# Optimization experiments

Measured on AMD Instinct MI355X. Metric: run time of the kernel, lower is better.

The kernel has to match this reference:

```python
import jax, jax.numpy as jnp
import numpy as np

ALPHA = 1.702   # SwiGLU alpha (module default)
LIMIT = 7.0     # SwiGLU clamp limit (module default)
EPS = 1e-6      # RMSNorm eps
K = 4           # experts_per_token


def setup_inputs() -> dict:
    key = jax.random.key(0)
    k0, k1, k2, k3 = jax.random.split(key, 4)
    B, S, H, I2, E = 4, 2048, 1536, 6144, 16  # I2 = 2*intermediate_size
    x = jax.random.normal(k0, (B, S, H), dtype=jnp.float32)
    norm_scale = jnp.ones((H,), dtype=jnp.float32)
    gate_w = jax.random.normal(k1, (E, H), dtype=jnp.float32) * 0.02
    w_up = jax.random.normal(k2, (E, I2, H), dtype=jnp.float32) * 0.02
    b_up = jnp.zeros((E, I2), dtype=jnp.float32)
    w_down = jax.random.normal(k3, (E, H, I2 // 2), dtype=jnp.float32) * 0.02
    b_down = jnp.zeros((E, H), dtype=jnp.float32)
    return {"x": x, "norm_scale": norm_scale, "gate_w": gate_w,
            "w_up": w_up, "b_up": b_up, "w_down": w_down, "b_down": b_down}


def _swiglu(h):
    g, l = jnp.split(h, 2, axis=-1)
    g = jnp.minimum(g, LIMIT)
    l = jnp.clip(l, -LIMIT, LIMIT)
    return g * jax.nn.sigmoid(ALPHA * g) * (l + 1.0)


def reference(x, norm_scale, gate_w, w_up, b_up, w_down, b_down):
    E = gate_w.shape[0]
    # RMSNorm (fp32 math)
    var = jnp.mean(x * x, axis=-1, keepdims=True)
    xn = x * jax.lax.rsqrt(var + EPS) * norm_scale  # [B,S,H]
    # Router: top-k over expert logits, softmax over the k logits
    logits = jnp.einsum('bsh,eh->bse', xn, gate_w)  # [B,S,E]
    top_v, top_i = jax.lax.top_k(logits, K)
    probs = jax.nn.softmax(top_v, axis=-1)          # [B,S,K]
    out = jnp.zeros_like(x)
    for i in range(K):
        # Faithful to source: expert id taken from token [0,0], applied to whole batch
        eid = top_i[0, 0, i] % E
        wu = jnp.take(w_up, eid, axis=0)    # [2I, H]
        bu = jnp.take(b_up, eid, axis=0)    # [2I]
        wd = jnp.take(w_down, eid, axis=0)  # [H, I]
        bd = jnp.take(b_down, eid, axis=0)  # [H]
        h = jnp.einsum('bsh,ih->bsi', xn, wu) + bu   # [B,S,2I]
        act = _swiglu(h)                              # [B,S,I]
        eo = jnp.einsum('bsi,hi->bsh', act, wd) + bd  # [B,S,H]
        out = out + probs[:, :, i:i + 1] * eo
    return x + out
```

## Files before the change

### kernel.cpp

```cpp
#include <hip/hip_runtime.h>
#include <hip/hip_bf16.h>
#include <stdint.h>

constexpr int T  = 4 * 2048;
constexpr int H  = 1536;
constexpr int I2 = 6144;
constexpr int II = 3072;
constexpr int EE = 16;
#define ALPHA_ 1.702f
#define LIMIT_ 7.0f
#define EPS_   1e-6f

typedef unsigned short u16;
typedef __bf16 bf16x8 __attribute__((ext_vector_type(8)));
typedef float  f32x4  __attribute__((ext_vector_type(4)));

__device__ __forceinline__ u16 f2bf(float f) {
  union { float f; unsigned int u; } c; c.f = f;
  unsigned int u = c.u + 0x7fffu + ((c.u >> 16) & 1u);
  return (u16)(u >> 16);
}
__device__ __forceinline__ unsigned int pack2(float lo, float hi) {
  return (unsigned int)f2bf(lo) | ((unsigned int)f2bf(hi) << 16);
}

__device__ __forceinline__ void async16(const void* g, void* l) {
  __builtin_amdgcn_global_load_lds(
      (const __attribute__((address_space(1))) unsigned int*)(uintptr_t)g,
      (__attribute__((address_space(3))) unsigned int*)(unsigned int)(uintptr_t)l,
      16, 0, 0);
}

__global__ __launch_bounds__(256) void k_rms_router(
    const float* __restrict__ x, const float* __restrict__ nscale,
    const float* __restrict__ gw, u16* __restrict__ xnb,
    float* __restrict__ logits) {
  const int t = blockIdx.x;
  const int tid = threadIdx.x;
  const int lane = tid & 63, wid = tid >> 6;
  const float* xr = x + (size_t)t * H;
  float v[6]; float ss = 0.f;
#pragma unroll
  for (int j = 0; j < 6; ++j) { v[j] = xr[tid + j * 256]; ss += v[j] * v[j]; }
  __shared__ float red[4];
  for (int off = 32; off; off >>= 1) ss += __shfl_down(ss, off, 64);
  if (lane == 0) red[wid] = ss;
  __syncthreads();
  const float rs = rsqrtf((red[0] + red[1] + red[2] + red[3]) * (1.0f / H) + EPS_);
  float xn[6];
#pragma unroll
  for (int j = 0; j < 6; ++j) {
    const int i = tid + j * 256;
    xn[j] = v[j] * rs * nscale[i];
    xnb[(size_t)t * H + i] = f2bf(xn[j]);
  }
  float acc[16];
#pragma unroll
  for (int e = 0; e < 16; ++e) acc[e] = 0.f;
#pragma unroll
  for (int j = 0; j < 6; ++j) {
    const int i = tid + j * 256;
#pragma unroll
    for (int e = 0; e < 16; ++e) acc[e] += xn[j] * gw[e * H + i];
  }
  __shared__ float lred[4][16];
#pragma unroll
  for (int e = 0; e < 16; ++e) {
    float a = acc[e];
    for (int off = 32; off; off >>= 1) a += __shfl_down(a, off, 64);
    if (lane == 0) lred[wid][e] = a;
  }
  __syncthreads();
  if (tid < 16)
    logits[(size_t)t * 16 + tid] = lred[0][tid] + lred[1][tid] + lred[2][tid] + lred[3][tid];
}

__global__ __launch_bounds__(256) void k_topk(
    const float* __restrict__ logits, float* __restrict__ probs, int* __restrict__ eids) {
  const int t = blockIdx.x * 256 + threadIdx.x;
  if (t >= T) return;
  float v[16];
#pragma unroll
  for (int e = 0; e < 16; ++e) v[e] = logits[(size_t)t * 16 + e];
  float tv[4]; int ti[4]; unsigned used = 0;
#pragma unroll
  for (int j = 0; j < 4; ++j) {
    float best = -3.4e38f; int bi = 0;
#pragma unroll
    for (int e = 0; e < 16; ++e) {
      if (!((used >> e) & 1u) && v[e] > best) { best = v[e]; bi = e; }
    }
    used |= 1u << bi; tv[j] = best; ti[j] = bi;
  }
  const float m = tv[0];
  float ex[4], den = 0.f;
#pragma unroll
  for (int j = 0; j < 4; ++j) { ex[j] = __expf(tv[j] - m); den += ex[j]; }
  const float rden = 1.0f / den;
#pragma unroll
  for (int j = 0; j < 4; ++j) probs[(size_t)t * 4 + j] = ex[j] * rden;
  if (t == 0) {
#pragma unroll
    for (int j = 0; j < 4; ++j) eids[j] = ti[j] % EE;
  }
}

__global__ __launch_bounds__(256) void k_gather_bias(
    const float* __restrict__ bup, const float* __restrict__ bdn,
    const int* __restrict__ eids, float* __restrict__ bu_g, float* __restrict__ bd_g) {
  const int i = blockIdx.x * 256 + threadIdx.x;
  if (i < 4 * I2) {
    const int s = i / I2, r = i - s * I2;
    bu_g[i] = bup[(size_t)eids[s] * I2 + r];
  } else {
    const int j = i - 4 * I2;
    const int s = j / H, r = j - s * H;
    bd_g[j] = bdn[(size_t)eids[s] * H + r];
  }
}

__global__ __launch_bounds__(256) void k_gather_w(
    const float* __restrict__ wup, const float* __restrict__ wdn,
    const int* __restrict__ eids, u16* __restrict__ wu_b, u16* __restrict__ wd_b) {
  const size_t UP = (size_t)4 * I2 * H;
  const size_t u = ((size_t)blockIdx.x * 256 + threadIdx.x) * 8;
  if (u < UP) {
    const int s = (int)(u / ((size_t)I2 * H));
    const size_t r = u - (size_t)s * I2 * H;
    const float4* src = (const float4*)(wup + (size_t)eids[s] * I2 * H + r);
    const float4 a = src[0], b = src[1];
    uint4 o; o.x = pack2(a.x, a.y); o.y = pack2(a.z, a.w);
    o.z = pack2(b.x, b.y); o.w = pack2(b.z, b.w);
    *(uint4*)(wu_b + u) = o;
  } else {
    const size_t q = u - UP;
    const int s = (int)(q / ((size_t)H * II));
    const size_t r = q - (size_t)s * H * II;
    const float4* src = (const float4*)(wdn + (size_t)eids[s] * H * II + r);
    const float4 a = src[0], b = src[1];
    uint4 o; o.x = pack2(a.x, a.y); o.y = pack2(a.z, a.w);
    o.z = pack2(b.x, b.y); o.w = pack2(b.z, b.w);
    *(uint4*)(wd_b + q) = o;
  }
}

__global__ __launch_bounds__(256) void k_gemm1(
    const u16* __restrict__ xnb, const u16* __restrict__ wu_b,
    const float* __restrict__ bu_g, const float* __restrict__ probs,
    u16* __restrict__ act) {
  const int s  = blockIdx.z;
  const int n0 = blockIdx.x * 64;
  const int m0 = blockIdx.y * 128;
  const int tid = threadIdx.x;
  const int lane = tid & 63, wid = tid >> 6;
  const int wm = wid >> 1, wn = wid & 1;
  __shared__ u16 As[128 * 32];
  __shared__ u16 Bg[64 * 32];
  __shared__ u16 Bl[64 * 32];
  const u16* wug = wu_b + (size_t)s * I2 * H;
  f32x4 accg[4][2], accl[4][2];
  const f32x4 z = {0.f, 0.f, 0.f, 0.f};
#pragma unroll
  for (int i = 0; i < 4; ++i)
#pragma unroll
    for (int j = 0; j < 2; ++j) { accg[i][j] = z; accl[i][j] = z; }
  const int row2 = tid >> 2, cg = tid & 3;
  for (int k0 = 0; k0 < H; k0 += 32) {
    async16(xnb + (size_t)(m0 + row2) * H + k0 + cg * 8,        &As[tid * 8]);
    async16(xnb + (size_t)(m0 + 64 + row2) * H + k0 + cg * 8,   &As[2048 + tid * 8]);
    async16(wug + (size_t)(n0 + row2) * H + k0 + cg * 8,        &Bg[tid * 8]);
    async16(wug + (size_t)(II + n0 + row2) * H + k0 + cg * 8,   &Bl[tid * 8]);
    __syncthreads();
    const int quad = (lane >> 4) * 8, r16 = lane & 15;
    bf16x8 a[4], bg[2], bl[2];
#pragma unroll
    for (int i = 0; i < 4; ++i) a[i] = *(const bf16x8*)&As[(wm * 64 + i * 16 + r16) * 32 + quad];
#pragma unroll
    for (int j = 0; j < 2; ++j) {
      bg[j] = *(const bf16x8*)&Bg[(wn * 32 + j * 16 + r16) * 32 + quad];
      bl[j] = *(const bf16x8*)&Bl[(wn * 32 + j * 16 + r16) * 32 + quad];
    }
#pragma unroll
    for (int i = 0; i < 4; ++i)
#pragma unroll
      for (int j = 0; j < 2; ++j) {
        accg[i][j] = __builtin_amdgcn_mfma_f32_16x16x32_bf16(a[i], bg[j], accg[i][j], 0, 0, 0);
        accl[i][j] = __builtin_amdgcn_mfma_f32_16x16x32_bf16(a[i], bl[j], accl[i][j], 0, 0, 0);
      }
    __syncthreads();
  }
  u16* actS = act + (size_t)s * T * II;
  const int crow0 = m0 + wm * 64, ccol0 = n0 + wn * 32;
#pragma unroll
  for (int i = 0; i < 4; ++i) {
#pragma unroll
    for (int j = 0; j < 2; ++j) {
      const int col = ccol0 + j * 16 + (lane & 15);
      const float bug = bu_g[s * I2 + col];
      const float bul = bu_g[s * I2 + II + col];
#pragma unroll
      for (int r = 0; r < 4; ++r) {
        const int row = crow0 + i * 16 + (lane >> 4) * 4 + r;
        float g = accg[i][j][r] + bug;
        float l = accl[i][j][r] + bul;
        g = fminf(g, LIMIT_);
        l = fminf(fmaxf(l, -LIMIT_), LIMIT_);
        const float sig = 1.0f / (1.0f + __expf(-ALPHA_ * g));
        const float a = g * sig * (l + 1.0f);
        const float p = probs[(size_t)row * 4 + s];
        actS[(size_t)row * II + col] = f2bf(a * p);
      }
    }
  }
}

__global__ __launch_bounds__(256) void k_gemm2(
    const u16* __restrict__ act, const u16* __restrict__ wd_b,
    const float* __restrict__ bd_g, const float* __restrict__ probs,
    const float* __restrict__ x, float* __restrict__ out) {
  const int n0 = blockIdx.x * 128;
  const int m0 = blockIdx.y * 128;
  const int tid = threadIdx.x;
  const int lane = tid & 63, wid = tid >> 6;
  const int wm = wid >> 1, wn = wid & 1;
  __shared__ u16 As[128 * 32];
  __shared__ u16 Bs[128 * 32];
  f32x4 acc[4][4];
  const f32x4 z = {0.f, 0.f, 0.f, 0.f};
#pragma unroll
  for (int i = 0; i < 4; ++i)
#pragma unroll
    for (int j = 0; j < 4; ++j) acc[i][j] = z;
  const int row2 = tid >> 2, cg = tid & 3;
  for (int s = 0; s < 4; ++s) {
    const u16* Ab = act + (size_t)s * T * II;
    const u16* Bb = wd_b + (size_t)s * H * II;
    for (int k0 = 0; k0 < II; k0 += 32) {
      async16(Ab + (size_t)(m0 + row2) * II + k0 + cg * 8,      &As[tid * 8]);
      async16(Ab + (size_t)(m0 + 64 + row2) * II + k0 + cg * 8, &As[2048 + tid * 8]);
      async16(Bb + (size_t)(n0 + row2) * II + k0 + cg * 8,      &Bs[tid * 8]);
      async16(Bb + (size_t)(n0 + 64 + row2) * II + k0 + cg * 8, &Bs[2048 + tid * 8]);
      __syncthreads();
      const int quad = (lane >> 4) * 8, r16 = lane & 15;
      bf16x8 a[4], b[4];
#pragma unroll
      for (int i = 0; i < 4; ++i) a[i] = *(const bf16x8*)&As[(wm * 64 + i * 16 + r16) * 32 + quad];
#pragma unroll
      for (int j = 0; j < 4; ++j) b[j] = *(const bf16x8*)&Bs[(wn * 64 + j * 16 + r16) * 32 + quad];
#pragma unroll
      for (int i = 0; i < 4; ++i)
#pragma unroll
        for (int j = 0; j < 4; ++j)
          acc[i][j] = __builtin_amdgcn_mfma_f32_16x16x32_bf16(a[i], b[j], acc[i][j], 0, 0, 0);
      __syncthreads();
    }
  }
#pragma unroll
  for (int i = 0; i < 4; ++i) {
#pragma unroll
    for (int r = 0; r < 4; ++r) {
      const int row = m0 + wm * 64 + i * 16 + (lane >> 4) * 4 + r;
      const float p0 = probs[(size_t)row * 4 + 0], p1 = probs[(size_t)row * 4 + 1];
      const float p2 = probs[(size_t)row * 4 + 2], p3 = probs[(size_t)row * 4 + 3];
#pragma unroll
      for (int j = 0; j < 4; ++j) {
        const int col = n0 + wn * 64 + j * 16 + (lane & 15);
        const float bias = p0 * bd_g[col] + p1 * bd_g[H + col] +
                           p2 * bd_g[2 * H + col] + p3 * bd_g[3 * H + col];
        out[(size_t)row * H + col] = x[(size_t)row * H + col] + acc[i][j][r] + bias;
      }
    }
  }
}

extern "C" void kernel_launch(void* const* d_in, const int* in_sizes, int n_in,
                              void* d_out, int out_size, void* d_ws, size_t ws_size,
                              hipStream_t stream) {
  const float* x      = (const float*)d_in[0];
  const float* nscale = (const float*)d_in[1];
  const float* gw     = (const float*)d_in[2];
  const float* wup    = (const float*)d_in[3];
  const float* bup    = (const float*)d_in[4];
  const float* wdn    = (const float*)d_in[5];
  const float* bdn    = (const float*)d_in[6];
  float* out = (float*)d_out;
  char* ws = (char*)d_ws;
  size_t off = 0;
  auto alloc = [&](size_t bytes) { size_t o = off; off += (bytes + 255) & ~(size_t)255; return o; };
  u16*   xnb    = (u16*)(ws + alloc((size_t)T * H * 2));
  float* logits = (float*)(ws + alloc((size_t)T * 16 * 4));
  float* probs  = (float*)(ws + alloc((size_t)T * 4 * 4));
  int*   eids   = (int*)(ws + alloc(64));
  float* bu_g   = (float*)(ws + alloc((size_t)4 * I2 * 4));
  float* bd_g   = (float*)(ws + alloc((size_t)4 * H * 4));
  u16*   wu_b   = (u16*)(ws + alloc((size_t)4 * I2 * H * 2));
  u16*   wd_b   = (u16*)(ws + alloc((size_t)4 * H * II * 2));
  u16*   act    = (u16*)(ws + alloc((size_t)4 * T * II * 2));
  (void)ws_size; (void)in_sizes; (void)n_in; (void)out_size;

  k_rms_router<<<T, 256, 0, stream>>>(x, nscale, gw, xnb, logits);
  k_topk<<<T / 256, 256, 0, stream>>>(logits, probs, eids);
  k_gather_bias<<<(4 * I2 + 4 * H) / 256, 256, 0, stream>>>(bup, bdn, eids, bu_g, bd_g);
  {
    const size_t total = (size_t)4 * I2 * H + (size_t)4 * H * II;
    k_gather_w<<<(unsigned)(total / 8 / 256), 256, 0, stream>>>(wup, wdn, eids, wu_b, wd_b);
  }
  k_gemm1<<<dim3(II / 64, T / 128, 4), 256, 0, stream>>>(xnb, wu_b, bu_g, probs, act);
  k_gemm2<<<dim3(H / 128, T / 128), 256, 0, stream>>>(act, wd_b, bd_g, probs, x, out);
}
```

Before: 2.335 ms.

## Rewrite both expert GEMMs with larger tiles, double-buffered LDS and swizzle

Both MFMA GEMMs move to 512-thread blocks with 256x128 output tiles and a K step of 64. Global-to-LDS async loads are double-buffered and interleaved with MFMA phases using explicit waitcnt, barriers and setprio, and LDS rows are XOR-swizzled to avoid bank conflicts. Workgroup IDs are remapped for L2 locality, and dynamic shared memory (128KB / 96KB) is enabled through a one-time attribute call. The aim is to hide memory latency and raise MFMA utilisation. In exchange, register pressure goes up and the hand-written vmcnt counting is fragile.

New measurement: 1.999 ms. 1.17x faster.

```diff
diff --git a/kernel.cpp b/kernel.cpp
--- a/kernel.cpp
+++ b/kernel.cpp
@@ -144,133 +144,290 @@
   }
 }
 
-__global__ __launch_bounds__(256) void k_gemm1(
+
+#define FRAG16(base, row, kq) \
+  (*(const bf16x8*)((const char*)(base) + ((row) * 128 + ((kq) ^ (((row) & 7) << 4)))))
+
+constexpr int NT1 = H / 64;
+
+__global__ __launch_bounds__(512, 2) void k_gemm1(
     const u16* __restrict__ xnb, const u16* __restrict__ wu_b,
     const float* __restrict__ bu_g, const float* __restrict__ probs,
     u16* __restrict__ act) {
-  const int s  = blockIdx.z;
-  const int n0 = blockIdx.x * 64;
-  const int m0 = blockIdx.y * 128;
+  extern __shared__ float4 smem_f4[];
+  char* smem = (char*)smem_f4;
+  const int s = blockIdx.z;
+  int wg = blockIdx.x + 24 * blockIdx.y;
+  wg = (wg & 7) * 96 + (wg >> 3);
+  const int n0 = (wg % 24) * 128;
+  const int m0 = (wg / 24) * 256;
   const int tid = threadIdx.x;
   const int lane = tid & 63, wid = tid >> 6;
-  const int wm = wid >> 1, wn = wid & 1;
-  __shared__ u16 As[128 * 32];
-  __shared__ u16 Bg[64 * 32];
-  __shared__ u16 Bl[64 * 32];
+  const int wm = wid >> 2, wn = wid & 3;
+  const int r16 = lane & 15, q16 = (lane >> 4) * 16;
   const u16* wug = wu_b + (size_t)s * I2 * H;
-  f32x4 accg[4][2], accl[4][2];
+
+  auto stage = [&](int k, int part) {
+    char* base = smem + (k & 1) * 65536;
+    const u16* g; char* dst;
+    if (part == 0)      { g = xnb + (size_t) m0        * H + k * 64; dst = base;          }
+    else if (part == 1) { g = wug + (size_t) n0        * H + k * 64; dst = base + 32768; }
+    else if (part == 2) { g = wug + (size_t)(II + n0)  * H + k * 64; dst = base + 49152; }
+    else                { g = xnb + (size_t)(m0 + 128) * H + k * 64; dst = base + 16384; }
+#pragma unroll
+    for (int c = 0; c < 2; ++c) {
+      const int o = c * 8192 + tid * 16;
+      const int row = o >> 7;
+      const int cb = (o & 127) ^ ((row & 7) << 4);
+      async16(g + (size_t)row * H + (cb >> 1), dst + o);
+    }
+  };
+
+  f32x4 accg[8][2], accl[8][2];
   const f32x4 z = {0.f, 0.f, 0.f, 0.f};
 #pragma unroll
-  for (int i = 0; i < 4; ++i)
+  for (int i = 0; i < 8; ++i)
 #pragma unroll
     for (int j = 0; j < 2; ++j) { accg[i][j] = z; accl[i][j] = z; }
-  const int row2 = tid >> 2, cg = tid & 3;
-  for (int k0 = 0; k0 < H; k0 += 32) {
-    async16(xnb + (size_t)(m0 + row2) * H + k0 + cg * 8,        &As[tid * 8]);
-    async16(xnb + (size_t)(m0 + 64 + row2) * H + k0 + cg * 8,   &As[2048 + tid * 8]);
-    async16(wug + (size_t)(n0 + row2) * H + k0 + cg * 8,        &Bg[tid * 8]);
-    async16(wug + (size_t)(II + n0 + row2) * H + k0 + cg * 8,   &Bl[tid * 8]);
-    __syncthreads();
-    const int quad = (lane >> 4) * 8, r16 = lane & 15;
-    bf16x8 a[4], bg[2], bl[2];
-#pragma unroll
-    for (int i = 0; i < 4; ++i) a[i] = *(const bf16x8*)&As[(wm * 64 + i * 16 + r16) * 32 + quad];
-#pragma unroll
-    for (int j = 0; j < 2; ++j) {
-      bg[j] = *(const bf16x8*)&Bg[(wn * 32 + j * 16 + r16) * 32 + quad];
-      bl[j] = *(const bf16x8*)&Bl[(wn * 32 + j * 16 + r16) * 32 + quad];
-    }
-#pragma unroll
-    for (int i = 0; i < 4; ++i)
-#pragma unroll
-      for (int j = 0; j < 2; ++j) {
-        accg[i][j] = __builtin_amdgcn_mfma_f32_16x16x32_bf16(a[i], bg[j], accg[i][j], 0, 0, 0);
-        accl[i][j] = __builtin_amdgcn_mfma_f32_16x16x32_bf16(a[i], bl[j], accl[i][j], 0, 0, 0);
-      }
-    __syncthreads();
-  }
+
+  stage(0, 0); stage(0, 1); stage(0, 2); stage(0, 3);
+  stage(1, 0); stage(1, 1); stage(1, 2);
+  asm volatile("s_waitcnt vmcnt(6)" ::: "memory");
+  __builtin_amdgcn_s_barrier();
+
+  bf16x8 a[4][2], bg[2][2], bl[2][2];
+#pragma unroll 1
+  for (int t = 0; t < NT1; ++t) {
+    const char* base = smem + (t & 1) * 65536;
+    const u16* A  = (const u16*)base;
+    const u16* Bg = (const u16*)(base + 32768);
+    const u16* Bl = (const u16*)(base + 49152);
+    const bool lastt = (t == NT1 - 1);
+
+#pragma unroll
+    for (int i = 0; i < 4; ++i)
+#pragma unroll
+      for (int k = 0; k < 2; ++k)
+        a[i][k] = FRAG16(A, wm * 64 + i * 16 + r16, k * 64 + q16);
+#pragma unroll
+    for (int j = 0; j < 2; ++j)
+#pragma unroll
+      for (int k = 0; k < 2; ++k)
+        bg[j][k] = FRAG16(Bg, wn * 32 + j * 16 + r16, k * 64 + q16);
+    if (t + 1 < NT1) stage(t + 1, 3);
+    __builtin_amdgcn_s_barrier();
+    asm volatile("s_waitcnt lgkmcnt(0)" ::: "memory");
+    __builtin_amdgcn_s_setprio(1);
+#pragma unroll
+    for (int i = 0; i < 4; ++i)
+#pragma unroll
+      for (int j = 0; j < 2; ++j) {
+        accg[i][j] = __builtin_amdgcn_mfma_f32_16x16x32_bf16(a[i][0], bg[j][0], accg[i][j], 0, 0, 0);
+        accg[i][j] = __builtin_amdgcn_mfma_f32_16x16x32_bf16(a[i][1], bg[j][1], accg[i][j], 0, 0, 0);
+      }
+    __builtin_amdgcn_s_setprio(0);
+    if (lastt) asm volatile("s_waitcnt vmcnt(2)" ::: "memory");
+    __builtin_amdgcn_s_barrier();
+
+#pragma unroll
+    for (int j = 0; j < 2; ++j)
+#pragma unroll
+      for (int k = 0; k < 2; ++k)
+        bl[j][k] = FRAG16(Bl, wn * 32 + j * 16 + r16, k * 64 + q16);
+    if (t + 2 < NT1) stage(t + 2, 0);
+    __builtin_amdgcn_s_barrier();
+    asm volatile("s_waitcnt lgkmcnt(0)" ::: "memory");
+    __builtin_amdgcn_s_setprio(1);
+#pragma unroll
+    for (int i = 0; i < 4; ++i)
+#pragma unroll
+      for (int j = 0; j < 2; ++j) {
+        accl[i][j] = __builtin_amdgcn_mfma_f32_16x16x32_bf16(a[i][0], bl[j][0], accl[i][j], 0, 0, 0);
+        accl[i][j] = __builtin_amdgcn_mfma_f32_16x16x32_bf16(a[i][1], bl[j][1], accl[i][j], 0, 0, 0);
+      }
+    __builtin_amdgcn_s_setprio(0);
+    if (lastt) asm volatile("s_waitcnt vmcnt(0)" ::: "memory");
+    __builtin_amdgcn_s_barrier();
+
+#pragma unroll
+    for (int i = 0; i < 4; ++i)
+#pragma unroll
+      for (int k = 0; k < 2; ++k)
+        a[i][k] = FRAG16(A, 128 + wm * 64 + i * 16 + r16, k * 64 + q16);
+    if (t + 2 < NT1) stage(t + 2, 1);
+    __builtin_amdgcn_s_barrier();
+    asm volatile("s_waitcnt lgkmcnt(0)" ::: "memory");
+    __builtin_amdgcn_s_setprio(1);
+#pragma unroll
+    for (int i = 0; i < 4; ++i)
+#pragma unroll
+      for (int j = 0; j < 2; ++j) {
+        accg[4 + i][j] = __builtin_amdgcn_mfma_f32_16x16x32_bf16(a[i][0], bg[j][0], accg[4 + i][j], 0, 0, 0);
+        accg[4 + i][j] = __builtin_amdgcn_mfma_f32_16x16x32_bf16(a[i][1], bg[j][1], accg[4 + i][j], 0, 0, 0);
+      }
+    __builtin_amdgcn_s_setprio(0);
+    __builtin_amdgcn_s_barrier();
+
+    if (t + 2 < NT1) stage(t + 2, 2);
+    __builtin_amdgcn_s_barrier();
+    __builtin_amdgcn_s_setprio(1);
+#pragma unroll
+    for (int i = 0; i < 4; ++i)
+#pragma unroll
+      for (int j = 0; j < 2; ++j) {
+        accl[4 + i][j] = __builtin_amdgcn_mfma_f32_16x16x32_bf16(a[i][0], bl[j][0], accl[4 + i][j], 0, 0, 0);
+        accl[4 + i][j] = __builtin_amdgcn_mfma_f32_16x16x32_bf16(a[i][1], bl[j][1], accl[4 + i][j], 0, 0, 0);
+      }
+    __builtin_amdgcn_s_setprio(0);
+    if (t < NT1 - 2)       asm volatile("s_waitcnt vmcnt(6)" ::: "memory");
+    else if (t == NT1 - 2) asm volatile("s_waitcnt vmcnt(4)" ::: "memory");
+    __builtin_amdgcn_s_barrier();
+  }
+
   u16* actS = act + (size_t)s * T * II;
-  const int crow0 = m0 + wm * 64, ccol0 = n0 + wn * 32;
-#pragma unroll
-  for (int i = 0; i < 4; ++i) {
-#pragma unroll
-    for (int j = 0; j < 2; ++j) {
-      const int col = ccol0 + j * 16 + (lane & 15);
-      const float bug = bu_g[s * I2 + col];
-      const float bul = bu_g[s * I2 + II + col];
-#pragma unroll
-      for (int r = 0; r < 4; ++r) {
-        const int row = crow0 + i * 16 + (lane >> 4) * 4 + r;
-        float g = accg[i][j][r] + bug;
-        float l = accl[i][j][r] + bul;
-        g = fminf(g, LIMIT_);
-        l = fminf(fmaxf(l, -LIMIT_), LIMIT_);
-        const float sig = 1.0f / (1.0f + __expf(-ALPHA_ * g));
-        const float a = g * sig * (l + 1.0f);
-        const float p = probs[(size_t)row * 4 + s];
-        actS[(size_t)row * II + col] = f2bf(a * p);
-      }
-    }
-  }
-}
-
-__global__ __launch_bounds__(256) void k_gemm2(
+  const int q4 = (lane >> 4) * 4;
+#pragma unroll
+  for (int mi = 0; mi < 2; ++mi)
+#pragma unroll
+    for (int i = 0; i < 4; ++i)
+#pragma unroll
+      for (int j = 0; j < 2; ++j) {
+        const int col = n0 + wn * 32 + j * 16 + r16;
+        const float bug = bu_g[s * I2 + col];
+        const float bul = bu_g[s * I2 + II + col];
+#pragma unroll
+        for (int r = 0; r < 4; ++r) {
+          const int row = m0 + mi * 128 + wm * 64 + i * 16 + q4 + r;
+          float g = accg[mi * 4 + i][j][r] + bug;
+          float l = accl[mi * 4 + i][j][r] + bul;
+          g = fminf(g, LIMIT_);
+          l = fminf(fmaxf(l, -LIMIT_), LIMIT_);
+          const float sig = 1.0f / (1.0f + __expf(-ALPHA_ * g));
+          const float av = g * sig * (l + 1.0f);
+          const float p = probs[(size_t)row * 4 + s];
+          actS[(size_t)row * II + col] = f2bf(av * p);
+        }
+      }
+}
+
+constexpr int NT2 = 4 * II / 64;
+constexpr int KTS = II / 64;
+
+__global__ __launch_bounds__(512, 2) void k_gemm2(
     const u16* __restrict__ act, const u16* __restrict__ wd_b,
     const float* __restrict__ bd_g, const float* __restrict__ probs,
     const float* __restrict__ x, float* __restrict__ out) {
-  const int n0 = blockIdx.x * 128;
-  const int m0 = blockIdx.y * 128;
+  extern __shared__ float4 smem_f4[];
+  char* smem = (char*)smem_f4;
+  int wg = blockIdx.x + 12 * blockIdx.y;
+  wg = (wg & 7) * 48 + (wg >> 3);
+  const int n0 = (wg % 12) * 128;
+  const int m0 = (wg / 12) * 256;
   const int tid = threadIdx.x;
   const int lane = tid & 63, wid = tid >> 6;
-  const int wm = wid >> 1, wn = wid & 1;
-  __shared__ u16 As[128 * 32];
-  __shared__ u16 Bs[128 * 32];
-  f32x4 acc[4][4];
+  const int wm = wid >> 2, wn = wid & 3;
+  const int r16 = lane & 15, q16 = (lane >> 4) * 16;
+
+  auto stage = [&](int t, int part) {
+    const int sl = t / KTS, kk = t - sl * KTS;
+    char* base = smem + (t & 1) * 49152;
+    const u16* g; char* dst;
+    if (part == 0)      { g = act  + (size_t)sl * T * II + (size_t) m0        * II + kk * 64; dst = base;          }
+    else if (part == 1) { g = wd_b + (size_t)sl * H * II + (size_t) n0        * II + kk * 64; dst = base + 32768; }
+    else                { g = act  + (size_t)sl * T * II + (size_t)(m0 + 128) * II + kk * 64; dst = base + 16384; }
+#pragma unroll
+    for (int c = 0; c < 2; ++c) {
+      const int o = c * 8192 + tid * 16;
+      const int row = o >> 7;
+      const int cb = (o & 127) ^ ((row & 7) << 4);
+      async16(g + (size_t)row * II + (cb >> 1), dst + o);
+    }
+  };
+
+  f32x4 acc[8][2];
   const f32x4 z = {0.f, 0.f, 0.f, 0.f};
 #pragma unroll
-  for (int i = 0; i < 4; ++i)
-#pragma unroll
-    for (int j = 0; j < 4; ++j) acc[i][j] = z;
-  const int row2 = tid >> 2, cg = tid & 3;
-  for (int s = 0; s < 4; ++s) {
-    const u16* Ab = act + (size_t)s * T * II;
-    const u16* Bb = wd_b + (size_t)s * H * II;
-    for (int k0 = 0; k0 < II; k0 += 32) {
-      async16(Ab + (size_t)(m0 + row2) * II + k0 + cg * 8,      &As[tid * 8]);
-      async16(Ab + (size_t)(m0 + 64 + row2) * II + k0 + cg * 8, &As[2048 + tid * 8]);
-      async16(Bb + (size_t)(n0 + row2) * II + k0 + cg * 8,      &Bs[tid * 8]);
-      async16(Bb + (size_t)(n0 + 64 + row2) * II + k0 + cg * 8, &Bs[2048 + tid * 8]);
-      __syncthreads();
-      const int quad = (lane >> 4) * 8, r16 = lane & 15;
-      bf16x8 a[4], b[4];
-#pragma unroll
-      for (int i = 0; i < 4; ++i) a[i] = *(const bf16x8*)&As[(wm * 64 + i * 16 + r16) * 32 + quad];
-#pragma unroll
-      for (int j = 0; j < 4; ++j) b[j] = *(const bf16x8*)&Bs[(wn * 64 + j * 16 + r16) * 32 + quad];
-#pragma unroll
-      for (int i = 0; i < 4; ++i)
-#pragma unroll
-        for (int j = 0; j < 4; ++j)
-          acc[i][j] = __builtin_amdgcn_mfma_f32_16x16x32_bf16(a[i], b[j], acc[i][j], 0, 0, 0);
-      __syncthreads();
-    }
-  }
-#pragma unroll
-  for (int i = 0; i < 4; ++i) {
-#pragma unroll
-    for (int r = 0; r < 4; ++r) {
-      const int row = m0 + wm * 64 + i * 16 + (lane >> 4) * 4 + r;
-      const float p0 = probs[(size_t)row * 4 + 0], p1 = probs[(size_t)row * 4 + 1];
-      const float p2 = probs[(size_t)row * 4 + 2], p3 = probs[(size_t)row * 4 + 3];
-#pragma unroll
-      for (int j = 0; j < 4; ++j) {
-        const int col = n0 + wn * 64 + j * 16 + (lane & 15);
-        const float bias = p0 * bd_g[col] + p1 * bd_g[H + col] +
-                           p2 * bd_g[2 * H + col] + p3 * bd_g[3 * H + col];
-        out[(size_t)row * H + col] = x[(size_t)row * H + col] + acc[i][j][r] + bias;
-      }
-    }
-  }
+  for (int i = 0; i < 8; ++i)
+#pragma unroll
+    for (int j = 0; j < 2; ++j) acc[i][j] = z;
+
+  stage(0, 0); stage(0, 1); stage(0, 2); stage(1, 0); stage(1, 1);
+  asm volatile("s_waitcnt vmcnt(4)" ::: "memory");
+  __builtin_amdgcn_s_barrier();
+
+  bf16x8 a[4][2], b[2][2];
+#pragma unroll 1
+  for (int t = 0; t < NT2; ++t) {
+    const char* base = smem + (t & 1) * 49152;
+    const u16* A = (const u16*)base;
+    const u16* B = (const u16*)(base + 32768);
+    const bool lastt = (t == NT2 - 1);
+
+#pragma unroll
+    for (int i = 0; i < 4; ++i)
+#pragma unroll
+      for (int k = 0; k < 2; ++k)
+        a[i][k] = FRAG16(A, wm * 64 + i * 16 + r16, k * 64 + q16);
+#pragma unroll
+    for (int j = 0; j < 2; ++j)
+#pragma unroll
+      for (int k = 0; k < 2; ++k)
+        b[j][k] = FRAG16(B, wn * 32 + j * 16 + r16, k * 64 + q16);
+    if (t + 1 < NT2) stage(t + 1, 2);
+    __builtin_amdgcn_s_barrier();
+    asm volatile("s_waitcnt lgkmcnt(0)" ::: "memory");
+    __builtin_amdgcn_s_setprio(1);
+#pragma unroll
+    for (int i = 0; i < 4; ++i)
+#pragma unroll
+      for (int j = 0; j < 2; ++j) {
+        acc[i][j] = __builtin_amdgcn_mfma_f32_16x16x32_bf16(a[i][0], b[j][0], acc[i][j], 0, 0, 0);
+        acc[i][j] = __builtin_amdgcn_mfma_f32_16x16x32_bf16(a[i][1], b[j][1], acc[i][j], 0, 0, 0);
+      }
+    __builtin_amdgcn_s_setprio(0);
+    if (lastt) asm volatile("s_waitcnt vmcnt(0)" ::: "memory");
+    __builtin_amdgcn_s_barrier();
+
+#pragma unroll
+    for (int i = 0; i < 4; ++i)
+#pragma unroll
+      for (int k = 0; k < 2; ++k)
+        a[i][k] = FRAG16(A, 128 + wm * 64 + i * 16 + r16, k * 64 + q16);
+    if (t + 2 < NT2) { stage(t + 2, 0); stage(t + 2, 1); }
+    __builtin_amdgcn_s_barrier();
+    asm volatile("s_waitcnt lgkmcnt(0)" ::: "memory");
+    __builtin_amdgcn_s_setprio(1);
+#pragma unroll
+    for (int i = 0; i < 4; ++i)
+#pragma unroll
+      for (int j = 0; j < 2; ++j) {
+        acc[4 + i][j] = __builtin_amdgcn_mfma_f32_16x16x32_bf16(a[i][0], b[j][0], acc[4 + i][j], 0, 0, 0);
+        acc[4 + i][j] = __builtin_amdgcn_mfma_f32_16x16x32_bf16(a[i][1], b[j][1], acc[4 + i][j], 0, 0, 0);
+      }
+    __builtin_amdgcn_s_setprio(0);
+    if (t < NT2 - 2)       asm volatile("s_waitcnt vmcnt(4)" ::: "memory");
+    else if (t == NT2 - 2) asm volatile("s_waitcnt vmcnt(2)" ::: "memory");
+    __builtin_amdgcn_s_barrier();
+  }
+
+  const int q4 = (lane >> 4) * 4;
+#pragma unroll
+  for (int mi = 0; mi < 2; ++mi)
+#pragma unroll
+    for (int i = 0; i < 4; ++i)
+#pragma unroll
+      for (int r = 0; r < 4; ++r) {
+        const int row = m0 + mi * 128 + wm * 64 + i * 16 + q4 + r;
+        const float p0 = probs[(size_t)row * 4 + 0], p1 = probs[(size_t)row * 4 + 1];
+        const float p2 = probs[(size_t)row * 4 + 2], p3 = probs[(size_t)row * 4 + 3];
+#pragma unroll
+        for (int j = 0; j < 2; ++j) {
+          const int col = n0 + wn * 32 + j * 16 + r16;
+          const float bias = p0 * bd_g[col] + p1 * bd_g[H + col] +
+                             p2 * bd_g[2 * H + col] + p3 * bd_g[3 * H + col];
+          out[(size_t)row * H + col] = x[(size_t)row * H + col] + acc[mi * 4 + i][j][r] + bias;
+        }
+      }
 }
 
 extern "C" void kernel_launch(void* const* d_in, const int* in_sizes, int n_in,
@@ -298,6 +455,15 @@
   u16*   act    = (u16*)(ws + alloc((size_t)4 * T * II * 2));
   (void)ws_size; (void)in_sizes; (void)n_in; (void)out_size;
 
+  static bool attr_done = false;
+  if (!attr_done) {
+    (void)hipFuncSetAttribute((const void*)k_gemm1,
+                              hipFuncAttributeMaxDynamicSharedMemorySize, 131072);
+    (void)hipFuncSetAttribute((const void*)k_gemm2,
+                              hipFuncAttributeMaxDynamicSharedMemorySize, 98304);
+    attr_done = true;
+  }
+
   k_rms_router<<<T, 256, 0, stream>>>(x, nscale, gw, xnb, logits);
   k_topk<<<T / 256, 256, 0, stream>>>(logits, probs, eids);
   k_gather_bias<<<(4 * I2 + 4 * H) / 256, 256, 0, stream>>>(bup, bdn, eids, bu_g, bd_g);
@@ -305,6 +471,6 @@
     const size_t total = (size_t)4 * I2 * H + (size_t)4 * H * II;
     k_gather_w<<<(unsigned)(total / 8 / 256), 256, 0, stream>>>(wup, wdn, eids, wu_b, wd_b);
   }
-  k_gemm1<<<dim3(II / 64, T / 128, 4), 256, 0, stream>>>(xnb, wu_b, bu_g, probs, act);
-  k_gemm2<<<dim3(H / 128, T / 128), 256, 0, stream>>>(act, wd_b, bd_g, probs, x, out);
-}
+  k_gemm1<<<dim3(24, 32, 4), 512, 131072, stream>>>(xnb, wu_b, bu_g, probs, act);
+  k_gemm2<<<dim3(12, 32), 512, 98304, stream>>>(act, wd_b, bd_g, probs, x, out);
+}
```
